# Performance work log

Hardware: AMD Instinct MI355X
Metric: run time of the kernel (lower is better)

The kernel has to match this reference:

```python
import jax, jax.numpy as jnp
import numpy as np

DIM = 256
HEADS = 8
DIM_HEAD = 64
INNER = HEADS * DIM_HEAD  # 512
SCALE = DIM_HEAD ** -0.5
EPS = 1e-5


def _layernorm(x, w, b):
    mu = jnp.mean(x, axis=-1, keepdims=True)
    var = jnp.var(x, axis=-1, keepdims=True)
    return (x - mu) * jax.lax.rsqrt(var + EPS) * w + b


def setup_inputs() -> dict:
    key = jax.random.key(0)
    ks = jax.random.split(key, 20)
    B, N, M, H, W = 8, 4096, 256, 64, 64
    s = 0.02
    inp = {
        "feat": jax.random.normal(ks[0], (B, N, DIM), jnp.float32),
        "center": jax.random.normal(ks[1], (B, M, DIM), jnp.float32),
        "pos": jax.random.normal(ks[2], (B, DIM, H, W), jnp.float32),
        "center_pos": jax.random.normal(ks[3], (B, M, DIM), jnp.float32),
        # projection weights stored [in, out] so y = x @ W
        "Wq": jax.random.normal(ks[4], (DIM, INNER), jnp.float32) * s,
        "Wk": jax.random.normal(ks[5], (DIM, INNER), jnp.float32) * s,
        "Wv1": jax.random.normal(ks[6], (DIM, INNER), jnp.float32) * s,
        "Wv2": jax.random.normal(ks[7], (DIM, INNER), jnp.float32) * s,
        "Wo1": jax.random.normal(ks[8], (INNER, DIM), jnp.float32) * s,
        "Wo2": jax.random.normal(ks[9], (INNER, DIM), jnp.float32) * s,
        "ln1_w": jnp.ones((DIM,), jnp.float32),
        "ln1_b": jnp.zeros((DIM,), jnp.float32),
        "ln2_w": jnp.ones((DIM,), jnp.float32),
        "ln2_b": jnp.zeros((DIM,), jnp.float32),
        "ffn1_W1": jax.random.normal(ks[10], (DIM, DIM), jnp.float32) * s,
        "ffn1_W2": jax.random.normal(ks[11], (DIM, DIM), jnp.float32) * s,
        "ffn1_b2": jnp.zeros((DIM,), jnp.float32),
        "ffn2_W1": jax.random.normal(ks[12], (DIM, DIM), jnp.float32) * s,
        "ffn2_W2": jax.random.normal(ks[13], (DIM, DIM), jnp.float32) * s,
        "ffn2_b2": jnp.zeros((DIM,), jnp.float32),
    }
    return inp


def reference(feat, center, pos, center_pos, Wq, Wk, Wv1, Wv2, Wo1, Wo2,
              ln1_w, ln1_b, ln2_w, ln2_b, ffn1_W1, ffn1_W2, ffn1_b2,
              ffn2_W1, ffn2_W2, ffn2_b2):
    B = feat.shape[0]
    # pos: [B, C, H, W] -> [B, N, C]
    pos_f = pos.reshape(B, DIM, -1).transpose(0, 2, 1)
    q = (feat + pos_f) @ Wq            # [B, N, INNER]
    k = (center + center_pos) @ Wk     # [B, M, INNER]
    v1 = feat @ Wv1                    # [B, N, INNER]
    v2 = center @ Wv2                  # [B, M, INNER]

    def split(x):  # [B, T, h*d] -> [B, h, T, d]
        return x.reshape(B, x.shape[1], HEADS, DIM_HEAD).transpose(0, 2, 1, 3)

    q, k, v1, v2 = split(q), split(k), split(v1), split(v2)
    attn = jnp.einsum("bhnd,bhmd->bhnm", q, k) * SCALE  # [B, h, N, M]
    attn1 = jax.nn.softmax(attn, axis=-2)  # over N (queries)
    attn2 = jax.nn.softmax(attn, axis=-1)  # over M (keys)
    out_feat = jnp.einsum("bhnm,bhmd->bhnd", attn2, v2)    # [B, h, N, d]
    out_center = jnp.einsum("bhnm,bhnd->bhmd", attn1, v1)  # [B, h, M, d]

    def merge(x):  # [B, h, T, d] -> [B, T, h*d]
        return x.transpose(0, 2, 1, 3).reshape(B, x.shape[2], INNER)

    out_feat = merge(out_feat) @ Wo1 + feat
    out_center = merge(out_center) @ Wo2 + center
    out_feat = _layernorm(out_feat, ln1_w, ln1_b)
    out_center = _layernorm(out_center, ln2_w, ln2_b)
    out_feat = jax.nn.relu(out_feat @ ffn1_W1) @ ffn1_W2 + ffn1_b2 + out_feat
    out_center = jax.nn.relu(out_center @ ffn2_W1) @ ffn2_W2 + ffn2_b2 + out_center
    return out_feat, out_center
```

## Files before the change

### kernel.cpp

```cpp
#include <hip/hip_runtime.h>

typedef __bf16 bf16;
typedef __bf16 bf16x4 __attribute__((ext_vector_type(4)));
typedef __bf16 bf16x8 __attribute__((ext_vector_type(8)));
typedef float f32x4 __attribute__((ext_vector_type(4)));

#define MFMA16(a, b, c) __builtin_amdgcn_mfma_f32_16x16x32_bf16(a, b, c, 0, 0, 0)

#define CEXP 0.18033688011112042f

struct WTArgs {
  const float* src[10];
  bf16* dst[10];
  int K[10];
  int N[10];
};

__global__ __launch_bounds__(256) void wtrans_kernel(WTArgs args) {
  const int z = blockIdx.z;
  const int K = args.K[z], N = args.N[z];
  const int k0 = blockIdx.x * 64, n0 = blockIdx.y * 64;
  if (k0 >= K || n0 >= N) return;
  __shared__ float t[64][65];
  const int tx = threadIdx.x & 63, ty = threadIdx.x >> 6;
  const float* __restrict__ src = args.src[z];
  bf16* __restrict__ dst = args.dst[z];
#pragma unroll
  for (int i = 0; i < 16; ++i)
    t[ty + i * 4][tx] = src[(size_t)(k0 + ty + i * 4) * N + n0 + tx];
  __syncthreads();
#pragma unroll
  for (int i = 0; i < 16; ++i)
    dst[(size_t)(n0 + ty + i * 4) * K + k0 + tx] = (bf16)t[tx][ty + i * 4];
}

__global__ __launch_bounds__(256) void prep_xq_kernel(
    const float* __restrict__ feat, const float* __restrict__ pos,
    bf16* __restrict__ xq) {
  const int n0 = blockIdx.x * 64;
  const int c0 = blockIdx.y * 64;
  const int b = blockIdx.z;
  __shared__ float t[64][65];
  const int tx = threadIdx.x & 63, ty = threadIdx.x >> 6;
#pragma unroll
  for (int i = 0; i < 16; ++i) {
    int c = ty + i * 4;
    t[c][tx] = pos[((size_t)b * 256 + c0 + c) * 4096 + n0 + tx];
  }
  __syncthreads();
#pragma unroll
  for (int i = 0; i < 16; ++i) {
    int n = ty + i * 4;
    size_t off = ((size_t)b * 4096 + n0 + n) * 256 + c0 + tx;
    xq[off] = (bf16)(feat[off] + t[tx][n]);
  }
}

__global__ __launch_bounds__(256) void addvec_kernel(
    const float* __restrict__ a, const float* __restrict__ b,
    bf16* __restrict__ o, int n4) {
  int i = blockIdx.x * 256 + threadIdx.x;
  if (i < n4) {
    f32x4 x = ((const f32x4*)a)[i];
    f32x4 y = ((const f32x4*)b)[i];
    bf16x4 z;
#pragma unroll
    for (int j = 0; j < 4; ++j) z[j] = (bf16)(x[j] + y[j]);
    ((bf16x4*)o)[i] = z;
  }
}

template <typename TA>
__device__ inline bf16x8 ldA8(const TA* p);
template <>
__device__ inline bf16x8 ldA8<bf16>(const bf16* p) {
  return *(const bf16x8*)p;
}
template <>
__device__ inline bf16x8 ldA8<float>(const float* p) {
  f32x4 u = *(const f32x4*)p;
  f32x4 v = *((const f32x4*)p + 1);
  bf16x8 o;
#pragma unroll
  for (int i = 0; i < 4; ++i) {
    o[i] = (bf16)u[i];
    o[4 + i] = (bf16)v[i];
  }
  return o;
}

template <int EPI, typename TO, typename TR, typename TA>
__global__ __launch_bounds__(256) void gemm_kernel(
    const TA* __restrict__ A, const bf16* __restrict__ BT,
    TO* __restrict__ C, const TR* __restrict__ resid,
    const float* __restrict__ bias, int M, int N, int K) {
  const int m0 = blockIdx.x * 128;
  const int n0 = blockIdx.y * 128;
  const int tid = threadIdx.x;
  const int lane = tid & 63;
  const int w = tid >> 6;
  const int wr = (w >> 1) * 64, wc = (w & 1) * 64;
  const int l15 = lane & 15, quad = lane >> 4;

  __shared__ bf16 Al[128 * 40];
  __shared__ bf16 Bl[128 * 40];

  f32x4 acc[4][4];
#pragma unroll
  for (int i = 0; i < 4; ++i)
#pragma unroll
    for (int j = 0; j < 4; ++j) acc[i][j] = (f32x4){0.f, 0.f, 0.f, 0.f};

  for (int k0 = 0; k0 < K; k0 += 32) {
#pragma unroll
    for (int c = 0; c < 2; ++c) {
      int idx = tid + c * 256;
      int row = idx >> 2;
      int ko = (idx & 3) * 8;
      *(bf16x8*)(Al + row * 40 + ko) =
          ldA8(A + (size_t)(m0 + row) * K + k0 + ko);
      *(bf16x8*)(Bl + row * 40 + ko) =
          *(const bf16x8*)(BT + (size_t)(n0 + row) * K + k0 + ko);
    }
    __syncthreads();
    bf16x8 fa[4], fb[4];
#pragma unroll
    for (int i = 0; i < 4; ++i) {
      fa[i] = *(const bf16x8*)(Al + (wr + i * 16 + l15) * 40 + quad * 8);
      fb[i] = *(const bf16x8*)(Bl + (wc + i * 16 + l15) * 40 + quad * 8);
    }
#pragma unroll
    for (int i = 0; i < 4; ++i)
#pragma unroll
      for (int j = 0; j < 4; ++j)
        acc[i][j] = MFMA16(fa[i], fb[j], acc[i][j]);
    __syncthreads();
  }

#pragma unroll
  for (int i = 0; i < 4; ++i) {
#pragma unroll
    for (int r = 0; r < 4; ++r) {
      int row = m0 + wr + i * 16 + quad * 4 + r;
      size_t rb = (size_t)row * N + n0 + wc;
#pragma unroll
      for (int j = 0; j < 4; ++j) {
        int col = j * 16 + l15;
        float v = acc[i][j][r];
        if constexpr (EPI == 1) v = fmaxf(v, 0.f);
        if constexpr (EPI == 2) v += (float)resid[rb + col];
        if constexpr (EPI == 3)
          v += bias[n0 + wc + col] + (float)resid[rb + col];
        C[rb + col] = (TO)v;
      }
    }
  }
}

__global__ __launch_bounds__(256) void attf_kernel(
    const bf16* q, const bf16* __restrict__ kk, const bf16* __restrict__ v1,
    const bf16* __restrict__ v2, bf16* af, float* __restrict__ acc_c,
    float* __restrict__ colsum) {
  const int nb = blockIdx.x;
  const int h = blockIdx.y;
  const int b = blockIdx.z;
  const int tid = threadIdx.x;
  const int lane = tid & 63;
  const int w = tid >> 6;
  const int l15 = lane & 15, quad = lane >> 4;

  __shared__ bf16 klds[64 * 72];
  __shared__ bf16 v2T[64 * 72];
  __shared__ bf16 v1T[64 * 72];
  __shared__ bf16 PT[64 * 72];
  __shared__ bf16 Pl[4][16 * 72];

  f32x4 oc2[16];
#pragma unroll
  for (int i = 0; i < 16; ++i) oc2[i] = (f32x4){0.f, 0.f, 0.f, 0.f};
  float cs[16];
#pragma unroll
  for (int i = 0; i < 16; ++i) cs[i] = 0.f;

  for (int ch = 0; ch < 8; ++ch) {
    int nrow = b * 4096 + nb * 512 + ch * 64 + w * 16 + l15;
    const bf16* qp = q + (size_t)nrow * 512 + h * 64 + quad * 8;
    bf16x8 a0 = *(const bf16x8*)(qp);
    bf16x8 a1 = *(const bf16x8*)(qp + 32);

    f32x4 o1[4];
#pragma unroll
    for (int i = 0; i < 4; ++i) o1[i] = (f32x4){0.f, 0.f, 0.f, 0.f};
    float rs[4] = {0.f, 0.f, 0.f, 0.f};

    for (int mq = 0; mq < 4; ++mq) {
      __syncthreads();
#pragma unroll
      for (int c = 0; c < 2; ++c) {
        int idx = tid + c * 256;
        int m = idx >> 3, dc = (idx & 7) * 8;
        *(bf16x8*)(klds + m * 72 + dc) = *(const bf16x8*)(
            kk + ((size_t)(b * 256 + mq * 64 + m)) * 512 + h * 64 + dc);
      }
#pragma unroll
      for (int c = 0; c < 16; ++c) {
        int idx = tid + c * 256;
        int m = idx >> 6, d = idx & 63;
        v2T[d * 72 + m] =
            v2[((size_t)(b * 256 + mq * 64 + m)) * 512 + h * 64 + d];
      }
      if (mq == 0) {
#pragma unroll
        for (int c = 0; c < 16; ++c) {
          int idx = tid + c * 256;
          int nl = idx >> 6, d = idx & 63;
          v1T[d * 72 + nl] = v1[((size_t)(b * 4096 + nb * 512 + ch * 64 + nl)) *
                                    512 + h * 64 + d];
        }
      }
      __syncthreads();

#pragma unroll
      for (int mt = 0; mt < 4; ++mt) {
        const bf16* kp = klds + (mt * 16 + l15) * 72 + quad * 8;
        bf16x8 b0 = *(const bf16x8*)(kp);
        bf16x8 b1 = *(const bf16x8*)(kp + 32);
        f32x4 s = (f32x4){0.f, 0.f, 0.f, 0.f};
        s = MFMA16(a0, b0, s);
        s = MFMA16(a1, b1, s);
        float e0 = exp2f(s[0] * CEXP);
        float e1 = exp2f(s[1] * CEXP);
        float e2 = exp2f(s[2] * CEXP);
        float e3 = exp2f(s[3] * CEXP);
        rs[0] += e0; rs[1] += e1; rs[2] += e2; rs[3] += e3;
        cs[mq * 4 + mt] += e0 + e1 + e2 + e3;
        Pl[w][(quad * 4 + 0) * 72 + mt * 16 + l15] = (bf16)e0;
        Pl[w][(quad * 4 + 1) * 72 + mt * 16 + l15] = (bf16)e1;
        Pl[w][(quad * 4 + 2) * 72 + mt * 16 + l15] = (bf16)e2;
        Pl[w][(quad * 4 + 3) * 72 + mt * 16 + l15] = (bf16)e3;
        bf16x4 ev;
        ev[0] = (bf16)e0; ev[1] = (bf16)e1; ev[2] = (bf16)e2; ev[3] = (bf16)e3;
        *(bf16x4*)(PT + (mt * 16 + l15) * 72 + w * 16 + quad * 4) = ev;
      }
      __syncthreads();

#pragma unroll
      for (int ks = 0; ks < 2; ++ks) {
        bf16x8 pa = *(const bf16x8*)(Pl[w] + l15 * 72 + ks * 32 + quad * 8);
#pragma unroll
        for (int dt = 0; dt < 4; ++dt) {
          bf16x8 vb =
              *(const bf16x8*)(v2T + (dt * 16 + l15) * 72 + ks * 32 + quad * 8);
          o1[dt] = MFMA16(pa, vb, o1[dt]);
        }
      }
#pragma unroll
      for (int ks = 0; ks < 2; ++ks) {
        bf16x8 pa2 =
            *(const bf16x8*)(PT + (w * 16 + l15) * 72 + ks * 32 + quad * 8);
#pragma unroll
        for (int dt = 0; dt < 4; ++dt) {
          bf16x8 vb =
              *(const bf16x8*)(v1T + (dt * 16 + l15) * 72 + ks * 32 + quad * 8);
          oc2[mq * 4 + dt] = MFMA16(pa2, vb, oc2[mq * 4 + dt]);
        }
      }
    }

    float inv[4];
#pragma unroll
    for (int r = 0; r < 4; ++r) {
      float v = rs[r];
      v += __shfl_xor(v, 1, 64);
      v += __shfl_xor(v, 2, 64);
      v += __shfl_xor(v, 4, 64);
      v += __shfl_xor(v, 8, 64);
      inv[r] = 1.f / v;
    }
#pragma unroll
    for (int dt = 0; dt < 4; ++dt) {
#pragma unroll
      for (int r = 0; r < 4; ++r) {
        int n = nb * 512 + ch * 64 + w * 16 + quad * 4 + r;
        af[((size_t)(b * 4096 + n)) * 512 + h * 64 + dt * 16 + l15] =
            (bf16)(o1[dt][r] * inv[r]);
      }
    }
  }

#pragma unroll
  for (int t = 0; t < 16; ++t) {
    float v = cs[t];
    v += __shfl_xor(v, 16, 64);
    v += __shfl_xor(v, 32, 64);
    if (quad == 0)
      atomicAdd(&colsum[(b * 8 + h) * 256 + (t >> 2) * 64 + (t & 3) * 16 + l15],
                v);
  }
  float* base = acc_c + ((size_t)(b * 8 + h)) * 256 * 64;
#pragma unroll
  for (int mq = 0; mq < 4; ++mq) {
#pragma unroll
    for (int dt = 0; dt < 4; ++dt) {
#pragma unroll
      for (int r = 0; r < 4; ++r) {
        int m = mq * 64 + w * 16 + quad * 4 + r;
        atomicAdd(base + m * 64 + dt * 16 + l15, oc2[mq * 4 + dt][r]);
      }
    }
  }
}

__global__ __launch_bounds__(256) void acm_kernel(
    const float* __restrict__ acc_c, const float* __restrict__ colsum,
    bf16* __restrict__ acm) {
  int idx = blockIdx.x * 256 + threadIdx.x;
  int d = idx & 63;
  int h = (idx >> 6) & 7;
  int m = (idx >> 9) & 255;
  int b = idx >> 17;
  float cv = colsum[(b * 8 + h) * 256 + m];
  float v = acc_c[(((size_t)(b * 8 + h)) * 256 + m) * 64 + d] / cv;
  acm[idx] = (bf16)v;
}

__global__ __launch_bounds__(256) void ln_kernel(
    const bf16* __restrict__ x, const float* __restrict__ wv,
    const float* __restrict__ bv, bf16* __restrict__ y, int rows) {
  int wave = threadIdx.x >> 6;
  int lane = threadIdx.x & 63;
  int row = blockIdx.x * 4 + wave;
  if (row >= rows) return;
  const bf16* xr = x + (size_t)row * 256;
  bf16x4 v = *(const bf16x4*)(xr + lane * 4);
  float f0 = v[0], f1 = v[1], f2 = v[2], f3 = v[3];
  float s = f0 + f1 + f2 + f3;
  float ss = f0 * f0 + f1 * f1 + f2 * f2 + f3 * f3;
#pragma unroll
  for (int m = 1; m < 64; m <<= 1) {
    s += __shfl_xor(s, m, 64);
    ss += __shfl_xor(ss, m, 64);
  }
  float mean = s * (1.f / 256.f);
  float var = ss * (1.f / 256.f) - mean * mean;
  float rstd = rsqrtf(var + 1e-5f);
  f32x4 wq = *(const f32x4*)(wv + lane * 4);
  f32x4 bq = *(const f32x4*)(bv + lane * 4);
  bf16x4 o;
  o[0] = (bf16)((f0 - mean) * rstd * wq[0] + bq[0]);
  o[1] = (bf16)((f1 - mean) * rstd * wq[1] + bq[1]);
  o[2] = (bf16)((f2 - mean) * rstd * wq[2] + bq[2]);
  o[3] = (bf16)((f3 - mean) * rstd * wq[3] + bq[3]);
  *(bf16x4*)(y + (size_t)row * 256 + lane * 4) = o;
}

extern "C" void kernel_launch(void* const* d_in, const int* in_sizes, int n_in,
                              void* d_out, int out_size, void* d_ws,
                              size_t ws_size, hipStream_t stream) {
  const float* feat = (const float*)d_in[0];
  const float* center = (const float*)d_in[1];
  const float* pos = (const float*)d_in[2];
  const float* cpos = (const float*)d_in[3];
  const float* Wq = (const float*)d_in[4];
  const float* Wk = (const float*)d_in[5];
  const float* Wv1 = (const float*)d_in[6];
  const float* Wv2 = (const float*)d_in[7];
  const float* Wo1 = (const float*)d_in[8];
  const float* Wo2 = (const float*)d_in[9];
  const float* ln1w = (const float*)d_in[10];
  const float* ln1b = (const float*)d_in[11];
  const float* ln2w = (const float*)d_in[12];
  const float* ln2b = (const float*)d_in[13];
  const float* f1W1 = (const float*)d_in[14];
  const float* f1W2 = (const float*)d_in[15];
  const float* f1b2 = (const float*)d_in[16];
  const float* f2W1 = (const float*)d_in[17];
  const float* f2W2 = (const float*)d_in[18];
  const float* f2b2 = (const float*)d_in[19];

  char* ws = (char*)d_ws;
  const size_t MB = 1024 * 1024;
  bf16* q_ = (bf16*)(ws + 0);
  bf16* af_ = q_;
  bf16* v1_ = (bf16*)(ws + 32 * MB);
  bf16* xq_ = (bf16*)(ws + 64 * MB);
  bf16* rf_ = xq_;
  bf16* k_ = (bf16*)(ws + 80 * MB);
  bf16* xk_ = (bf16*)(ws + 82 * MB);
  bf16* rc_ = xk_;
  bf16* v2_ = (bf16*)(ws + 83 * MB);
  bf16* acm_ = v2_;
  float* acc_ = (float*)(ws + 85 * MB);
  float* colsum_ = (float*)(ws + 89 * MB);
  bf16* wt_ = (bf16*)(ws + 89 * MB + 65536);
  bf16* yf_ = q_;
  bf16* tf_ = (bf16*)(ws + 16 * MB);
  bf16* yc_ = (bf16*)(ws + 92 * MB);
  bf16* tc_ = (bf16*)(ws + 93 * MB);

  bf16* WqT = wt_;
  bf16* WkT = WqT + 131072;
  bf16* Wv1T = WkT + 131072;
  bf16* Wv2T = Wv1T + 131072;
  bf16* Wo1T = Wv2T + 131072;
  bf16* Wo2T = Wo1T + 131072;
  bf16* f1W1T = Wo2T + 131072;
  bf16* f1W2T = f1W1T + 65536;
  bf16* f2W1T = f1W2T + 65536;
  bf16* f2W2T = f2W1T + 65536;

  float* out_feat = (float*)d_out;
  float* out_center = out_feat + (size_t)8 * 4096 * 256;

  WTArgs wa;
  const float* srcs[10] = {Wq, Wk, Wv1, Wv2, Wo1, Wo2, f1W1, f1W2, f2W1, f2W2};
  bf16* dsts[10] = {WqT, WkT, Wv1T, Wv2T, Wo1T, Wo2T, f1W1T, f1W2T, f2W1T, f2W2T};
  int Ks[10] = {256, 256, 256, 256, 512, 512, 256, 256, 256, 256};
  int Ns[10] = {512, 512, 512, 512, 256, 256, 256, 256, 256, 256};
  for (int i = 0; i < 10; ++i) {
    wa.src[i] = srcs[i];
    wa.dst[i] = dsts[i];
    wa.K[i] = Ks[i];
    wa.N[i] = Ns[i];
  }

  wtrans_kernel<<<dim3(8, 8, 10), 256, 0, stream>>>(wa);
  prep_xq_kernel<<<dim3(64, 4, 8), 256, 0, stream>>>(feat, pos, xq_);
  addvec_kernel<<<dim3(512), 256, 0, stream>>>(center, cpos, xk_, 131072);
  hipMemsetAsync(ws + 85 * MB, 0, 4 * MB + 65536, stream);

  gemm_kernel<0, bf16, bf16, bf16><<<dim3(256, 4), 256, 0, stream>>>(
      xq_, WqT, q_, nullptr, nullptr, 32768, 512, 256);
  gemm_kernel<0, bf16, bf16, bf16><<<dim3(16, 4), 256, 0, stream>>>(
      xk_, WkT, k_, nullptr, nullptr, 2048, 512, 256);
  gemm_kernel<0, bf16, bf16, float><<<dim3(256, 4), 256, 0, stream>>>(
      feat, Wv1T, v1_, nullptr, nullptr, 32768, 512, 256);
  gemm_kernel<0, bf16, bf16, float><<<dim3(16, 4), 256, 0, stream>>>(
      center, Wv2T, v2_, nullptr, nullptr, 2048, 512, 256);

  attf_kernel<<<dim3(8, 8, 8), 256, 0, stream>>>(q_, k_, v1_, v2_, af_, acc_,
                                                 colsum_);
  acm_kernel<<<dim3(4096), 256, 0, stream>>>(acc_, colsum_, acm_);

  gemm_kernel<2, bf16, float, bf16><<<dim3(256, 2), 256, 0, stream>>>(
      af_, Wo1T, rf_, feat, nullptr, 32768, 256, 512);
  ln_kernel<<<dim3(8192), 256, 0, stream>>>(rf_, ln1w, ln1b, yf_, 32768);
  gemm_kernel<1, bf16, bf16, bf16><<<dim3(256, 2), 256, 0, stream>>>(
      yf_, f1W1T, tf_, nullptr, nullptr, 32768, 256, 256);
  gemm_kernel<3, float, bf16, bf16><<<dim3(256, 2), 256, 0, stream>>>(
      tf_, f1W2T, out_feat, yf_, f1b2, 32768, 256, 256);

  gemm_kernel<2, bf16, float, bf16><<<dim3(16, 2), 256, 0, stream>>>(
      acm_, Wo2T, rc_, center, nullptr, 2048, 256, 512);
  ln_kernel<<<dim3(512), 256, 0, stream>>>(rc_, ln2w, ln2b, yc_, 2048);
  gemm_kernel<1, bf16, bf16, bf16><<<dim3(16, 2), 256, 0, stream>>>(
      yc_, f2W1T, tc_, nullptr, nullptr, 2048, 256, 256);
  gemm_kernel<3, float, bf16, bf16><<<dim3(16, 2), 256, 0, stream>>>(
      tc_, f2W2T, out_center, yc_, f2b2, 2048, 256, 256);
}
```

Before: 439.2 us.

## Store V transposed from GEMM, async LDS loads, transposed MFMA for P^T, finer attention grid

The V1/V2 projection GEMMs now write their outputs in a per-head transposed layout, so the attention kernel loads its V tiles with vectorized row copies instead of scalar transposing gathers. The GEMM stages B (and bf16 A) tiles with global_load_lds direct-to-LDS loads into unpadded tiles. The attention kernel computes the transposed score tile with extra MFMAs and a second exp instead of writing P^T via a strided scatter, and halves the rows per block to double the grid. Unpadded LDS rows may add bank conflicts, and the extra MFMA/exp work adds compute.

```diff
diff --git a/kernel.cpp b/kernel.cpp
--- a/kernel.cpp
+++ b/kernel.cpp
@@ -8,6 +8,12 @@
 #define MFMA16(a, b, c) __builtin_amdgcn_mfma_f32_16x16x32_bf16(a, b, c, 0, 0, 0)
 
 #define CEXP 0.18033688011112042f
+
+__device__ inline void gload16(const bf16* g, bf16* l) {
+  __builtin_amdgcn_global_load_lds(
+      (const __attribute__((address_space(1))) unsigned int*)g,
+      (__attribute__((address_space(3))) unsigned int*)l, 16, 0, 0);
+}
 
 struct WTArgs {
   const float* src[10];
@@ -70,14 +76,7 @@
   }
 }
 
-template <typename TA>
-__device__ inline bf16x8 ldA8(const TA* p);
-template <>
-__device__ inline bf16x8 ldA8<bf16>(const bf16* p) {
-  return *(const bf16x8*)p;
-}
-template <>
-__device__ inline bf16x8 ldA8<float>(const float* p) {
+__device__ inline bf16x8 ldA8f(const float* p) {
   f32x4 u = *(const f32x4*)p;
   f32x4 v = *((const f32x4*)p + 1);
   bf16x8 o;
@@ -93,7 +92,7 @@
 __global__ __launch_bounds__(256) void gemm_kernel(
     const TA* __restrict__ A, const bf16* __restrict__ BT,
     TO* __restrict__ C, const TR* __restrict__ resid,
-    const float* __restrict__ bias, int M, int N, int K) {
+    const float* __restrict__ bias, int M, int N, int K, int shT) {
   const int m0 = blockIdx.x * 128;
   const int n0 = blockIdx.y * 128;
   const int tid = threadIdx.x;
@@ -101,9 +100,10 @@
   const int w = tid >> 6;
   const int wr = (w >> 1) * 64, wc = (w & 1) * 64;
   const int l15 = lane & 15, quad = lane >> 4;
-
-  __shared__ bf16 Al[128 * 40];
-  __shared__ bf16 Bl[128 * 40];
+  constexpr bool A_BF16 = (sizeof(TA) == 2);
+
+  __shared__ bf16 Al[128 * 32];
+  __shared__ bf16 Bl[128 * 32];
 
   f32x4 acc[4][4];
 #pragma unroll
@@ -114,20 +114,33 @@
   for (int k0 = 0; k0 < K; k0 += 32) {
 #pragma unroll
     for (int c = 0; c < 2; ++c) {
-      int idx = tid + c * 256;
-      int row = idx >> 2;
-      int ko = (idx & 3) * 8;
-      *(bf16x8*)(Al + row * 40 + ko) =
-          ldA8(A + (size_t)(m0 + row) * K + k0 + ko);
-      *(bf16x8*)(Bl + row * 40 + ko) =
-          *(const bf16x8*)(BT + (size_t)(n0 + row) * K + k0 + ko);
+      int r0 = w * 32 + c * 16;
+      gload16(BT + (size_t)(n0 + r0 + (lane >> 2)) * K + k0 + (lane & 3) * 8,
+              Bl + r0 * 32);
+    }
+    if constexpr (A_BF16) {
+#pragma unroll
+      for (int c = 0; c < 2; ++c) {
+        int r0 = w * 32 + c * 16;
+        gload16(A + (size_t)(m0 + r0 + (lane >> 2)) * K + k0 + (lane & 3) * 8,
+                Al + r0 * 32);
+      }
+    } else {
+#pragma unroll
+      for (int c = 0; c < 2; ++c) {
+        int idx = tid + c * 256;
+        int row = idx >> 2;
+        int ko = (idx & 3) * 8;
+        *(bf16x8*)(Al + row * 32 + ko) =
+            ldA8f((const float*)A + (size_t)(m0 + row) * K + k0 + ko);
+      }
     }
     __syncthreads();
     bf16x8 fa[4], fb[4];
 #pragma unroll
     for (int i = 0; i < 4; ++i) {
-      fa[i] = *(const bf16x8*)(Al + (wr + i * 16 + l15) * 40 + quad * 8);
-      fb[i] = *(const bf16x8*)(Bl + (wc + i * 16 + l15) * 40 + quad * 8);
+      fa[i] = *(const bf16x8*)(Al + (wr + i * 16 + l15) * 32 + quad * 8);
+      fb[i] = *(const bf16x8*)(Bl + (wc + i * 16 + l15) * 32 + quad * 8);
     }
 #pragma unroll
     for (int i = 0; i < 4; ++i)
@@ -145,21 +158,28 @@
       size_t rb = (size_t)row * N + n0 + wc;
 #pragma unroll
       for (int j = 0; j < 4; ++j) {
-        int col = j * 16 + l15;
+        int col = n0 + wc + j * 16 + l15;
         float v = acc[i][j][r];
         if constexpr (EPI == 1) v = fmaxf(v, 0.f);
-        if constexpr (EPI == 2) v += (float)resid[rb + col];
+        if constexpr (EPI == 2) v += (float)resid[rb + j * 16 + l15];
         if constexpr (EPI == 3)
-          v += bias[n0 + wc + col] + (float)resid[rb + col];
-        C[rb + col] = (TO)v;
+          v += bias[col] + (float)resid[rb + j * 16 + l15];
+        if constexpr (EPI == 4) {
+          int bb = row >> shT;
+          int tt = row & ((1 << shT) - 1);
+          C[((((size_t)bb * 8 + (col >> 6)) * 64 + (col & 63)) << shT) + tt] =
+              (TO)v;
+        } else {
+          C[rb + j * 16 + l15] = (TO)v;
+        }
       }
     }
   }
 }
 
 __global__ __launch_bounds__(256) void attf_kernel(
-    const bf16* q, const bf16* __restrict__ kk, const bf16* __restrict__ v1,
-    const bf16* __restrict__ v2, bf16* af, float* __restrict__ acc_c,
+    const bf16* q, const bf16* __restrict__ kk, const bf16* __restrict__ v1t,
+    const bf16* __restrict__ v2t, bf16* af, float* __restrict__ acc_c,
     float* __restrict__ colsum) {
   const int nb = blockIdx.x;
   const int h = blockIdx.y;
@@ -175,6 +195,10 @@
   __shared__ bf16 PT[64 * 72];
   __shared__ bf16 Pl[4][16 * 72];
 
+  const size_t bh = (size_t)(b * 8 + h);
+  const bf16* v1tb = v1t + bh * 64 * 4096;
+  const bf16* v2tb = v2t + bh * 64 * 256;
+
   f32x4 oc2[16];
 #pragma unroll
   for (int i = 0; i < 16; ++i) oc2[i] = (f32x4){0.f, 0.f, 0.f, 0.f};
@@ -182,8 +206,9 @@
 #pragma unroll
   for (int i = 0; i < 16; ++i) cs[i] = 0.f;
 
-  for (int ch = 0; ch < 8; ++ch) {
-    int nrow = b * 4096 + nb * 512 + ch * 64 + w * 16 + l15;
+  for (int ch = 0; ch < 4; ++ch) {
+    const int nbase = nb * 256 + ch * 64;
+    int nrow = b * 4096 + nbase + w * 16 + l15;
     const bf16* qp = q + (size_t)nrow * 512 + h * 64 + quad * 8;
     bf16x8 a0 = *(const bf16x8*)(qp);
     bf16x8 a1 = *(const bf16x8*)(qp + 32);
@@ -203,19 +228,19 @@
             kk + ((size_t)(b * 256 + mq * 64 + m)) * 512 + h * 64 + dc);
       }
 #pragma unroll
-      for (int c = 0; c < 16; ++c) {
+      for (int c = 0; c < 2; ++c) {
         int idx = tid + c * 256;
-        int m = idx >> 6, d = idx & 63;
-        v2T[d * 72 + m] =
-            v2[((size_t)(b * 256 + mq * 64 + m)) * 512 + h * 64 + d];
+        int d = idx >> 3, mc = (idx & 7) * 8;
+        *(bf16x8*)(v2T + d * 72 + mc) =
+            *(const bf16x8*)(v2tb + (size_t)d * 256 + mq * 64 + mc);
       }
       if (mq == 0) {
 #pragma unroll
-        for (int c = 0; c < 16; ++c) {
+        for (int c = 0; c < 2; ++c) {
           int idx = tid + c * 256;
-          int nl = idx >> 6, d = idx & 63;
-          v1T[d * 72 + nl] = v1[((size_t)(b * 4096 + nb * 512 + ch * 64 + nl)) *
-                                    512 + h * 64 + d];
+          int d = idx >> 3, nc = (idx & 7) * 8;
+          *(bf16x8*)(v1T + d * 72 + nc) =
+              *(const bf16x8*)(v1tb + (size_t)d * 4096 + nbase + nc);
         }
       }
       __syncthreads();
@@ -228,6 +253,9 @@
         f32x4 s = (f32x4){0.f, 0.f, 0.f, 0.f};
         s = MFMA16(a0, b0, s);
         s = MFMA16(a1, b1, s);
+        f32x4 st = (f32x4){0.f, 0.f, 0.f, 0.f};
+        st = MFMA16(b0, a0, st);
+        st = MFMA16(b1, a1, st);
         float e0 = exp2f(s[0] * CEXP);
         float e1 = exp2f(s[1] * CEXP);
         float e2 = exp2f(s[2] * CEXP);
@@ -238,9 +266,10 @@
         Pl[w][(quad * 4 + 1) * 72 + mt * 16 + l15] = (bf16)e1;
         Pl[w][(quad * 4 + 2) * 72 + mt * 16 + l15] = (bf16)e2;
         Pl[w][(quad * 4 + 3) * 72 + mt * 16 + l15] = (bf16)e3;
-        bf16x4 ev;
-        ev[0] = (bf16)e0; ev[1] = (bf16)e1; ev[2] = (bf16)e2; ev[3] = (bf16)e3;
-        *(bf16x4*)(PT + (mt * 16 + l15) * 72 + w * 16 + quad * 4) = ev;
+#pragma unroll
+        for (int r = 0; r < 4; ++r)
+          PT[(mt * 16 + quad * 4 + r) * 72 + w * 16 + l15] =
+              (bf16)exp2f(st[r] * CEXP);
       }
       __syncthreads();
 
@@ -281,7 +310,7 @@
     for (int dt = 0; dt < 4; ++dt) {
 #pragma unroll
       for (int r = 0; r < 4; ++r) {
-        int n = nb * 512 + ch * 64 + w * 16 + quad * 4 + r;
+        int n = nbase + w * 16 + quad * 4 + r;
         af[((size_t)(b * 4096 + n)) * 512 + h * 64 + dt * 16 + l15] =
             (bf16)(o1[dt][r] * inv[r]);
       }
@@ -297,7 +326,7 @@
       atomicAdd(&colsum[(b * 8 + h) * 256 + (t >> 2) * 64 + (t & 3) * 16 + l15],
                 v);
   }
-  float* base = acc_c + ((size_t)(b * 8 + h)) * 256 * 64;
+  float* base = acc_c + bh * 256 * 64;
 #pragma unroll
   for (int mq = 0; mq < 4; ++mq) {
 #pragma unroll
@@ -382,14 +411,14 @@
   const size_t MB = 1024 * 1024;
   bf16* q_ = (bf16*)(ws + 0);
   bf16* af_ = q_;
-  bf16* v1_ = (bf16*)(ws + 32 * MB);
+  bf16* v1t_ = (bf16*)(ws + 32 * MB);
   bf16* xq_ = (bf16*)(ws + 64 * MB);
   bf16* rf_ = xq_;
   bf16* k_ = (bf16*)(ws + 80 * MB);
   bf16* xk_ = (bf16*)(ws + 82 * MB);
   bf16* rc_ = xk_;
-  bf16* v2_ = (bf16*)(ws + 83 * MB);
-  bf16* acm_ = v2_;
+  bf16* v2t_ = (bf16*)(ws + 83 * MB);
+  bf16* acm_ = v2t_;
   float* acc_ = (float*)(ws + 85 * MB);
   float* colsum_ = (float*)(ws + 89 * MB);
   bf16* wt_ = (bf16*)(ws + 89 * MB + 65536);
@@ -430,31 +459,31 @@
   hipMemsetAsync(ws + 85 * MB, 0, 4 * MB + 65536, stream);
 
   gemm_kernel<0, bf16, bf16, bf16><<<dim3(256, 4), 256, 0, stream>>>(
-      xq_, WqT, q_, nullptr, nullptr, 32768, 512, 256);
+      xq_, WqT, q_, nullptr, nullptr, 32768, 512, 256, 0);
   gemm_kernel<0, bf16, bf16, bf16><<<dim3(16, 4), 256, 0, stream>>>(
-      xk_, WkT, k_, nullptr, nullptr, 2048, 512, 256);
-  gemm_kernel<0, bf16, bf16, float><<<dim3(256, 4), 256, 0, stream>>>(
-      feat, Wv1T, v1_, nullptr, nullptr, 32768, 512, 256);
-  gemm_kernel<0, bf16, bf16, float><<<dim3(16, 4), 256, 0, stream>>>(
-      center, Wv2T, v2_, nullptr, nullptr, 2048, 512, 256);
-
-  attf_kernel<<<dim3(8, 8, 8), 256, 0, stream>>>(q_, k_, v1_, v2_, af_, acc_,
-                                                 colsum_);
+      xk_, WkT, k_, nullptr, nullptr, 2048, 512, 256, 0);
+  gemm_kernel<4, bf16, bf16, float><<<dim3(256, 4), 256, 0, stream>>>(
+      feat, Wv1T, v1t_, nullptr, nullptr, 32768, 512, 256, 12);
+  gemm_kernel<4, bf16, bf16, float><<<dim3(16, 4), 256, 0, stream>>>(
+      center, Wv2T, v2t_, nullptr, nullptr, 2048, 512, 256, 8);
+
+  attf_kernel<<<dim3(16, 8, 8), 256, 0, stream>>>(q_, k_, v1t_, v2t_, af_,
+                                                  acc_, colsum_);
   acm_kernel<<<dim3(4096), 256, 0, stream>>>(acc_, colsum_, acm_);
 
   gemm_kernel<2, bf16, float, bf16><<<dim3(256, 2), 256, 0, stream>>>(
-      af_, Wo1T, rf_, feat, nullptr, 32768, 256, 512);
+      af_, Wo1T, rf_, feat, nullptr, 32768, 256, 512, 0);
   ln_kernel<<<dim3(8192), 256, 0, stream>>>(rf_, ln1w, ln1b, yf_, 32768);
   gemm_kernel<1, bf16, bf16, bf16><<<dim3(256, 2), 256, 0, stream>>>(
-      yf_, f1W1T, tf_, nullptr, nullptr, 32768, 256, 256);
+      yf_, f1W1T, tf_, nullptr, nullptr, 32768, 256, 256, 0);
   gemm_kernel<3, float, bf16, bf16><<<dim3(256, 2), 256, 0, stream>>>(
-      tf_, f1W2T, out_feat, yf_, f1b2, 32768, 256, 256);
+      tf_, f1W2T, out_feat, yf_, f1b2, 32768, 256, 256, 0);
 
   gemm_kernel<2, bf16, float, bf16><<<dim3(16, 2), 256, 0, stream>>>(
-      acm_, Wo2T, rc_, center, nullptr, 2048, 256, 512);
+      acm_, Wo2T, rc_, center, nullptr, 2048, 256, 512, 0);
   ln_kernel<<<dim3(512), 256, 0, stream>>>(rc_, ln2w, ln2b, yc_, 2048);
   gemm_kernel<1, bf16, bf16, bf16><<<dim3(16, 2), 256, 0, stream>>>(
-      yc_, f2W1T, tc_, nullptr, nullptr, 2048, 256, 256);
+      yc_, f2W1T, tc_, nullptr, nullptr, 2048, 256, 256, 0);
   gemm_kernel<3, float, bf16, bf16><<<dim3(16, 2), 256, 0, stream>>>(
-      tc_, f2W2T, out_center, yc_, f2b2, 2048, 256, 256);
-}
+      tc_, f2W2T, out_center, yc_, f2b2, 2048, 256, 256, 0);
+}
```

Result: slower. 562.7 us (+28.1%).
